# Kernel tuning notes

Hardware: AMD Instinct MI355X
Metric: run time of the kernel (lower is better)

Reference implementation:

```python
import jax, jax.numpy as jnp
import numpy as np

N = 50000
NEG_SLOPE = 0.2


def add_self_loops(edge_index, n):
    loop = jnp.arange(n, dtype=edge_index.dtype)
    return jnp.concatenate([edge_index, jnp.stack([loop, loop])], axis=1)


def gatv2_conv(x, edge_index, Wl, bl, Wr, br, att, bias):
    """PyG GATv2Conv (share_weights=False, concat=True, add_self_loops applied by caller).
    x: [N, Fin]; edge_index: [2, E] with row0=src(j), row1=dst(i); att: [H, D].
    Returns (out [N, H*D], alpha [E, H])."""
    src, dst = edge_index[0], edge_index[1]
    H, D = att.shape
    n = x.shape[0]
    xl = (x @ Wl + bl).reshape(n, H, D)   # source-side transform
    xr = (x @ Wr + br).reshape(n, H, D)   # target-side transform
    e = jax.nn.leaky_relu(xl[src] + xr[dst], NEG_SLOPE)        # [E, H, D]
    logit = jnp.einsum('ehd,hd->eh', e, att)                    # [E, H]
    # segment softmax over edges grouped by target node
    lmax = jax.ops.segment_max(logit, dst, num_segments=n)      # [N, H]
    ex = jnp.exp(logit - lmax[dst])
    denom = jax.ops.segment_sum(ex, dst, num_segments=n)
    alpha = ex / denom[dst]                                     # [E, H]
    out = jax.ops.segment_sum(alpha[:, :, None] * xl[src], dst, num_segments=n)  # [N, H, D]
    return out.reshape(n, H * D) + bias, alpha


def setup_inputs() -> dict:
    key = jax.random.key(0)
    ks = jax.random.split(key, 16)
    E = 400000
    x = jax.random.normal(ks[0], (N, 23), dtype=jnp.float32)
    edge_index = jax.random.randint(ks[1], (2, E), 0, N, dtype=jnp.int64)
    H1, D1 = 8, 64
    F1 = H1 * D1  # 512
    s = 0.1
    return {
        'x': x,
        'edge_index': edge_index,
        'Wl1': jax.random.normal(ks[2], (23, F1), dtype=jnp.float32) * s,
        'bl1': jnp.zeros((F1,), jnp.float32),
        'Wr1': jax.random.normal(ks[3], (23, F1), dtype=jnp.float32) * s,
        'br1': jnp.zeros((F1,), jnp.float32),
        'att1': jax.random.normal(ks[4], (H1, D1), dtype=jnp.float32) * s,
        'bias1': jnp.zeros((F1,), jnp.float32),
        'Wl2': jax.random.normal(ks[5], (F1, 1), dtype=jnp.float32) * s,
        'bl2': jnp.zeros((1,), jnp.float32),
        'Wr2': jax.random.normal(ks[6], (F1, 1), dtype=jnp.float32) * s,
        'br2': jnp.zeros((1,), jnp.float32),
        'att2': jax.random.normal(ks[7], (1, 1), dtype=jnp.float32) * s,
        'bias2': jnp.zeros((1,), jnp.float32),
    }


def reference(x, edge_index, Wl1, bl1, Wr1, br1, att1, bias1,
              Wl2, bl2, Wr2, br2, att2, bias2):
    ei = add_self_loops(edge_index, N)
    h, _ = gatv2_conv(x, ei, Wl1, bl1, Wr1, br1, att1, bias1)
    h = jax.nn.relu(h)
    h, alpha = gatv2_conv(h, ei, Wl2, bl2, Wr2, br2, att2, bias2)
    return h, alpha
```

## Files before the change

### kernel.cpp

```cpp
#include <hip/hip_runtime.h>
#include <math.h>

#define NN 50000
#define E0 400000
#define EE 450000
#define FF 512
#define G1 2048
#define NPB 25
#define EPB 220
#define WAVES_TOTAL (G1 * 4)
#define MAXD 64
#define LOG2E 1.44269504f

typedef _Float16 h2 __attribute__((ext_vector_type(2)));

__device__ __forceinline__ h2 uas_h2(unsigned u) { union { unsigned u; h2 h; } c; c.u = u; return c.h; }
__device__ __forceinline__ unsigned h2as_u(h2 h) { union { unsigned u; h2 h; } c; c.h = h; return c.u; }
__device__ __forceinline__ unsigned packh(float a, float b) {
    h2 hh = { (_Float16)a, (_Float16)b };
    return h2as_u(hh);
}
__device__ __forceinline__ float leaky(float v) { return fmaxf(v, 0.2f * v); }

template<int CTRL>
__device__ __forceinline__ float dppadd(float v) {
    int s = __builtin_amdgcn_update_dpp(0, __float_as_int(v), CTRL, 0xF, 0xF, true);
    return v + __int_as_float(s);
}

__global__ __launch_bounds__(256) void k_predeg(
    const float* __restrict__ x,
    const float* __restrict__ Wl1, const float* __restrict__ bl1,
    const float* __restrict__ Wr1, const float* __restrict__ br1,
    const int* __restrict__ ei,
    unsigned short* __restrict__ xlq, float* __restrict__ xlsc,
    unsigned* __restrict__ xrh,
    int* __restrict__ cnt, int* __restrict__ src_sl)
{
    __shared__ unsigned sxh[NPB * 12];
    __shared__ float swm[2][4];
    int b = blockIdx.x, t = threadIdx.x;
    int l = t & 63, w = t >> 6;

    {
        int e0 = b * EPB;
        int e1 = e0 + EPB; if (e1 > EE) e1 = EE;
        for (int e = e0 + t; e < e1; e += 256) {
            int src, dst;
            if (e < E0) { src = ei[e]; dst = ei[E0 + e]; }
            else        { src = e - E0; dst = src; }
            int p = atomicAdd(&cnt[dst], 1);
            if (p < MAXD) src_sl[(size_t)dst * MAXD + p] = src;
        }
    }

    int i0 = b * NPB;
    int i1 = i0 + NPB; if (i1 > NN) i1 = NN;
    int nnod = i1 - i0;
    for (int k = t; k < nnod * 12; k += 256) {
        int n = k / 12, j = k - n * 12;
        const float* row = x + (size_t)(i0 + n) * 23;
        float f0 = row[2 * j];
        float f1 = (2 * j + 1 < 23) ? row[2 * j + 1] : 0.f;
        sxh[n * 12 + j] = packh(f0, f1);
    }

    int c0 = 2 * t, c1 = 2 * t + 1;
    h2 wl0[12], wl1[12], wr0[12], wr1[12];
#pragma unroll
    for (int j = 0; j < 12; j++) {
        int r0 = 2 * j, r1 = 2 * j + 1;
        float a, b2;
        a = Wl1[r0 * FF + c0]; b2 = (r1 < 23) ? Wl1[r1 * FF + c0] : 0.f;
        wl0[j] = (h2){ (_Float16)a, (_Float16)b2 };
        a = Wl1[r0 * FF + c1]; b2 = (r1 < 23) ? Wl1[r1 * FF + c1] : 0.f;
        wl1[j] = (h2){ (_Float16)a, (_Float16)b2 };
        a = Wr1[r0 * FF + c0]; b2 = (r1 < 23) ? Wr1[r1 * FF + c0] : 0.f;
        wr0[j] = (h2){ (_Float16)a, (_Float16)b2 };
        a = Wr1[r0 * FF + c1]; b2 = (r1 < 23) ? Wr1[r1 * FF + c1] : 0.f;
        wr1[j] = (h2){ (_Float16)a, (_Float16)b2 };
    }
    float bl0 = bl1[c0], bl1s = bl1[c1];
    float br0 = br1[c0], br1s = br1[c1];
    __syncthreads();

    const uint4* S = (const uint4*)sxh;
    for (int n = 0; n < nnod; n++) {
        uint4 xa = S[n * 3 + 0];
        uint4 xb = S[n * 3 + 1];
        uint4 xc = S[n * 3 + 2];
        h2 xv[12] = { uas_h2(xa.x), uas_h2(xa.y), uas_h2(xa.z), uas_h2(xa.w),
                      uas_h2(xb.x), uas_h2(xb.y), uas_h2(xb.z), uas_h2(xb.w),
                      uas_h2(xc.x), uas_h2(xc.y), uas_h2(xc.z), uas_h2(xc.w) };
        float al0 = bl0, al1 = bl1s, ar0 = br0, ar1 = br1s;
#pragma unroll
        for (int j = 0; j < 12; j++) {
            al0 = __builtin_amdgcn_fdot2(wl0[j], xv[j], al0, false);
            al1 = __builtin_amdgcn_fdot2(wl1[j], xv[j], al1, false);
            ar0 = __builtin_amdgcn_fdot2(wr0[j], xv[j], ar0, false);
            ar1 = __builtin_amdgcn_fdot2(wr1[j], xv[j], ar1, false);
        }
        xrh[(size_t)(i0 + n) * 256 + t] = packh(ar0, ar1);
        float ml = fmaxf(fabsf(al0), fabsf(al1));
#pragma unroll
        for (int o = 32; o > 0; o >>= 1) ml = fmaxf(ml, __shfl_xor(ml, o, 64));
        if (l == 0) swm[n & 1][w] = ml;
        __syncthreads();
        float rml = fmaxf(fmaxf(swm[n & 1][0], swm[n & 1][1]),
                          fmaxf(swm[n & 1][2], swm[n & 1][3]));
        rml = fmaxf(rml, 1e-8f);
        float qil = 127.f / rml;
        int q0 = (int)rintf(fminf(fmaxf(al0 * qil, -127.f), 127.f)) + 128;
        int q1 = (int)rintf(fminf(fmaxf(al1 * qil, -127.f), 127.f)) + 128;
        xlq[(size_t)(i0 + n) * 256 + t] =
            (unsigned short)((q0 & 0xFF) | ((q1 & 0xFF) << 8));
        if (t == 0) xlsc[i0 + n] = rml * (1.f / 127.f);
    }
}

__global__ __launch_bounds__(256) void k_layer1(
    const unsigned char* __restrict__ xlq, const float* __restrict__ xlsc,
    const uint4* __restrict__ xrh,
    const float* __restrict__ att, const float* __restrict__ bias1,
    const float* __restrict__ Wl2, const float* __restrict__ bl2,
    const float* __restrict__ Wr2, const float* __restrict__ br2,
    const int* __restrict__ cnt, const int* __restrict__ src_sl,
    float* __restrict__ xl2, float* __restrict__ xr2)
{
    int t = threadIdx.x;
    int l = t & 63;
    int wid = blockIdx.x * 4 + (t >> 6);

    float4 atA = ((const float4*)att)[2 * l];
    float4 atB = ((const float4*)att)[2 * l + 1];
    h2 a6_0 = { (_Float16)(0.6f * LOG2E * atA.x), (_Float16)(0.6f * LOG2E * atA.y) };
    h2 a6_1 = { (_Float16)(0.6f * LOG2E * atA.z), (_Float16)(0.6f * LOG2E * atA.w) };
    h2 a6_2 = { (_Float16)(0.6f * LOG2E * atB.x), (_Float16)(0.6f * LOG2E * atB.y) };
    h2 a6_3 = { (_Float16)(0.6f * LOG2E * atB.z), (_Float16)(0.6f * LOG2E * atB.w) };
    h2 a4_0 = { (_Float16)(0.4f * LOG2E * atA.x), (_Float16)(0.4f * LOG2E * atA.y) };
    h2 a4_1 = { (_Float16)(0.4f * LOG2E * atA.z), (_Float16)(0.4f * LOG2E * atA.w) };
    h2 a4_2 = { (_Float16)(0.4f * LOG2E * atB.x), (_Float16)(0.4f * LOG2E * atB.y) };
    h2 a4_3 = { (_Float16)(0.4f * LOG2E * atB.z), (_Float16)(0.4f * LOG2E * atB.w) };
    const h2 cm1152 = { (_Float16)(-1152.f), (_Float16)(-1152.f) };
    float bl2v = bl2[0], br2v = br2[0];

    for (int i = wid; i < NN; i += WAVES_TOTAL) {
        uint4 xq = xrh[(size_t)i * 64 + l];
        h2 xp0 = uas_h2(xq.x), xp1 = uas_h2(xq.y), xp2 = uas_h2(xq.z), xp3 = uas_h2(xq.w);

        float s = 0.f;
        h2 A0 = { 0, 0 }, A1 = { 0, 0 }, A2 = { 0, 0 }, A3 = { 0, 0 };

        int dg = cnt[i]; if (dg > MAXD) dg = MAXD;
        int myj = (l < dg) ? src_sl[(size_t)i * MAXD + l] : 0;

        int j0 = __builtin_amdgcn_readlane(myj, 0);
        uint2 r0 = *(const uint2*)(xlq + (size_t)j0 * 512 + 8 * l);
        float S0 = xlsc[j0];
        uint2 r1 = r0; float S1 = S0;
        if (dg > 1) {
            int j1 = __builtin_amdgcn_readlane(myj, 1);
            r1 = *(const uint2*)(xlq + (size_t)j1 * 512 + 8 * l);
            S1 = xlsc[j1];
        }

        for (int p = 0; p < dg; p++) {
            uint2 rn = r0; float Sn = S0;
            if (p + 2 < dg) {
                int jn = __builtin_amdgcn_readlane(myj, p + 2);
                rn = *(const uint2*)(xlq + (size_t)jn * 512 + 8 * l);
                Sn = xlsc[jn];
            }

            unsigned w0u = __builtin_amdgcn_perm(r0.x, 0x64646464u, 0x00050004u);
            unsigned w1u = __builtin_amdgcn_perm(r0.x, 0x64646464u, 0x00070006u);
            unsigned w2u = __builtin_amdgcn_perm(r0.y, 0x64646464u, 0x00050004u);
            unsigned w3u = __builtin_amdgcn_perm(r0.y, 0x64646464u, 0x00070006u);
            h2 qq0 = uas_h2(w0u) + cm1152, qq1 = uas_h2(w1u) + cm1152;
            h2 qq2 = uas_h2(w2u) + cm1152, qq3 = uas_h2(w3u) + cm1152;
            _Float16 Sh = (_Float16)S0;
            h2 Ss = { Sh, Sh };
            h2 v0 = qq0 * Ss, v1 = qq1 * Ss, v2 = qq2 * Ss, v3 = qq3 * Ss;
            h2 t0 = v0 + xp0, t1 = v1 + xp1, t2 = v2 + xp2, t3 = v3 + xp3;
            h2 b0 = uas_h2(h2as_u(t0) & 0x7fff7fffu);
            h2 b1 = uas_h2(h2as_u(t1) & 0x7fff7fffu);
            h2 b2 = uas_h2(h2as_u(t2) & 0x7fff7fffu);
            h2 b3 = uas_h2(h2as_u(t3) & 0x7fff7fffu);
            float part = 0.f;
            part = __builtin_amdgcn_fdot2(a6_0, t0, part, false);
            part = __builtin_amdgcn_fdot2(a4_0, b0, part, false);
            part = __builtin_amdgcn_fdot2(a6_1, t1, part, false);
            part = __builtin_amdgcn_fdot2(a4_1, b1, part, false);
            part = __builtin_amdgcn_fdot2(a6_2, t2, part, false);
            part = __builtin_amdgcn_fdot2(a4_2, b2, part, false);
            part = __builtin_amdgcn_fdot2(a6_3, t3, part, false);
            part = __builtin_amdgcn_fdot2(a4_3, b3, part, false);
            part = dppadd<0xB1>(part);
            part = dppadd<0x4E>(part);
            part = dppadd<0x141>(part);
            float wv = exp2f(part);
            s += wv;
            _Float16 wh = (_Float16)wv;
            h2 w2h = { wh, wh };
            A0 += w2h * v0;
            A1 += w2h * v1;
            A2 += w2h * v2;
            A3 += w2h * v3;
            r0 = r1; S0 = S1; r1 = rn; S1 = Sn;
        }

        float inv = 1.f / s;
        float4 bA = ((const float4*)bias1)[2 * l];
        float4 bB = ((const float4*)bias1)[2 * l + 1];
        float h0 = fmaxf(fmaf((float)A0[0], inv, bA.x), 0.f);
        float h1 = fmaxf(fmaf((float)A0[1], inv, bA.y), 0.f);
        float h2v = fmaxf(fmaf((float)A1[0], inv, bA.z), 0.f);
        float h3 = fmaxf(fmaf((float)A1[1], inv, bA.w), 0.f);
        float h4 = fmaxf(fmaf((float)A2[0], inv, bB.x), 0.f);
        float h5 = fmaxf(fmaf((float)A2[1], inv, bB.y), 0.f);
        float h6 = fmaxf(fmaf((float)A3[0], inv, bB.z), 0.f);
        float h7 = fmaxf(fmaf((float)A3[1], inv, bB.w), 0.f);

        float4 wlA = ((const float4*)Wl2)[2 * l];
        float4 wlB = ((const float4*)Wl2)[2 * l + 1];
        float4 wrA = ((const float4*)Wr2)[2 * l];
        float4 wrB = ((const float4*)Wr2)[2 * l + 1];
        float pl = h0 * wlA.x + h1 * wlA.y + h2v * wlA.z + h3 * wlA.w
                 + h4 * wlB.x + h5 * wlB.y + h6 * wlB.z + h7 * wlB.w;
        float pr = h0 * wrA.x + h1 * wrA.y + h2v * wrA.z + h3 * wrA.w
                 + h4 * wrB.x + h5 * wrB.y + h6 * wrB.z + h7 * wrB.w;
        pl = dppadd<0xB1>(pl);  pr = dppadd<0xB1>(pr);
        pl = dppadd<0x4E>(pl);  pr = dppadd<0x4E>(pr);
        pl = dppadd<0x141>(pl); pr = dppadd<0x141>(pr);
        pl = dppadd<0x140>(pl); pr = dppadd<0x140>(pr);
        pl += __shfl_xor(pl, 16, 64);  pr += __shfl_xor(pr, 16, 64);
        pl += __shfl_xor(pl, 32, 64);  pr += __shfl_xor(pr, 32, 64);
        if (l == 0) {
            xl2[i] = pl + bl2v;
            xr2[i] = pr + br2v;
        }
    }
}

__global__ void k_layer2a(const float* __restrict__ xl2, const float* __restrict__ xr2,
                          const float* __restrict__ att2, const float* __restrict__ bias2,
                          const int* __restrict__ cnt, const int* __restrict__ src_sl,
                          float* __restrict__ out, float* __restrict__ invs)
{
    int i = blockIdx.x * blockDim.x + threadIdx.x;
    if (i >= NN) return;
    int dg = cnt[i]; if (dg > MAXD) dg = MAXD;
    const int* sp = src_sl + (size_t)i * MAXD;
    float xri = xr2[i];
    float a2l = att2[0] * LOG2E;
    float s = 0.f, num = 0.f;
    for (int p = 0; p < dg; p++) {
        float v = xl2[sp[p]];
        float w = exp2f(leaky(v + xri) * a2l);
        s += w;
        num = fmaf(w, v, num);
    }
    out[i] = num / s + bias2[0];
    invs[i] = 1.f / s;
}

__global__ void k_layer2b(const float* __restrict__ xl2, const float* __restrict__ xr2,
                          const float* __restrict__ att2, const int* __restrict__ ei,
                          const float* __restrict__ invs, float* __restrict__ out)
{
    int e = blockIdx.x * blockDim.x + threadIdx.x;
    if (e >= EE) return;
    int src, dst;
    if (e < E0) { src = ei[e]; dst = ei[E0 + e]; }
    else        { src = e - E0; dst = src; }
    float a2l = att2[0] * LOG2E;
    float lg = leaky(xl2[src] + xr2[dst]) * a2l;
    out[NN + e] = exp2f(lg) * invs[dst];
}

extern "C" void kernel_launch(void* const* d_in, const int* in_sizes, int n_in,
                              void* d_out, int out_size, void* d_ws, size_t ws_size,
                              hipStream_t stream)
{
    const float* x     = (const float*)d_in[0];
    const int*   ei    = (const int*)d_in[1];
    const float* Wl1   = (const float*)d_in[2];
    const float* bl1   = (const float*)d_in[3];
    const float* Wr1   = (const float*)d_in[4];
    const float* br1   = (const float*)d_in[5];
    const float* att1  = (const float*)d_in[6];
    const float* bias1 = (const float*)d_in[7];
    const float* Wl2   = (const float*)d_in[8];
    const float* bl2   = (const float*)d_in[9];
    const float* Wr2   = (const float*)d_in[10];
    const float* br2   = (const float*)d_in[11];
    const float* att2  = (const float*)d_in[12];
    const float* bias2 = (const float*)d_in[13];
    float* out = (float*)d_out;

    char* ws = (char*)d_ws;
    unsigned short* xlq = (unsigned short*)ws; ws += (size_t)NN * 512;
    float* xlsc    = (float*)ws;    ws += (size_t)NN * 4;
    unsigned* xrh  = (unsigned*)ws; ws += (size_t)NN * 256 * 4;
    float* xl2     = (float*)ws;    ws += (size_t)NN * 4;
    float* xr2     = (float*)ws;    ws += (size_t)NN * 4;
    float* invs    = (float*)ws;    ws += (size_t)NN * 4;
    int* cnt       = (int*)ws;      ws += (size_t)NN * 4;
    int* src_sl    = (int*)ws;      ws += (size_t)NN * MAXD * 4;

    hipMemsetAsync(cnt, 0, (size_t)NN * 4, stream);

    k_predeg<<<G1, 256, 0, stream>>>(x, Wl1, bl1, Wr1, br1, ei, xlq, xlsc, xrh,
                                     cnt, src_sl);
    k_layer1<<<G1, 256, 0, stream>>>((const unsigned char*)xlq, xlsc,
                                     (const uint4*)xrh,
                                     att1, bias1, Wl2, bl2, Wr2, br2,
                                     cnt, src_sl, xl2, xr2);
    k_layer2a<<<(NN + 255) / 256, 256, 0, stream>>>(xl2, xr2, att2, bias2,
                                                    cnt, src_sl, out, invs);
    k_layer2b<<<(EE + 255) / 256, 256, 0, stream>>>(xl2, xr2, att2, ei, invs, out);
}
```

Measured before the change: 238.0 us.

## Batch per-node quantization sync, deepen gather prefetch, fold dequant into FMA

In the pre-degree kernel, the per-node __syncthreads used for the absmax reduction is replaced by a single barrier after all nodes. The unquantized fp16 values and per-wave maxima are staged in shared memory and quantized in a second pass. In layer1 the neighbour-row prefetch goes from two rows ahead to three, to hide more gather latency. The int8 dequantization (q-1152)*S is folded into one packed FMA q*S + (-1152*S). This costs about 25 KB of extra LDS per block and more registers, and the fp16 rounding of the folded constant slightly changes numerics.

```diff
diff --git a/kernel.cpp b/kernel.cpp
--- a/kernel.cpp
+++ b/kernel.cpp
@@ -38,7 +38,8 @@
     int* __restrict__ cnt, int* __restrict__ src_sl)
 {
     __shared__ unsigned sxh[NPB * 12];
-    __shared__ float swm[2][4];
+    __shared__ unsigned sal[NPB * 256];
+    __shared__ float swm[NPB * 4];
     int b = blockIdx.x, t = threadIdx.x;
     int l = t & 63, w = t >> 6;
 
@@ -101,20 +102,25 @@
             ar1 = __builtin_amdgcn_fdot2(wr1[j], xv[j], ar1, false);
         }
         xrh[(size_t)(i0 + n) * 256 + t] = packh(ar0, ar1);
+        sal[n * 256 + t] = packh(al0, al1);
         float ml = fmaxf(fabsf(al0), fabsf(al1));
 #pragma unroll
         for (int o = 32; o > 0; o >>= 1) ml = fmaxf(ml, __shfl_xor(ml, o, 64));
-        if (l == 0) swm[n & 1][w] = ml;
-        __syncthreads();
-        float rml = fmaxf(fmaxf(swm[n & 1][0], swm[n & 1][1]),
-                          fmaxf(swm[n & 1][2], swm[n & 1][3]));
-        rml = fmaxf(rml, 1e-8f);
-        float qil = 127.f / rml;
-        int q0 = (int)rintf(fminf(fmaxf(al0 * qil, -127.f), 127.f)) + 128;
-        int q1 = (int)rintf(fminf(fmaxf(al1 * qil, -127.f), 127.f)) + 128;
+        if (l == 0) swm[n * 4 + w] = ml;
+    }
+    __syncthreads();
+
+    for (int n = 0; n < nnod; n++) {
+        float rm = fmaxf(fmaxf(swm[n * 4 + 0], swm[n * 4 + 1]),
+                         fmaxf(swm[n * 4 + 2], swm[n * 4 + 3]));
+        rm = fmaxf(rm, 1e-8f);
+        float qi = 127.f / rm;
+        h2 alp = uas_h2(sal[n * 256 + t]);
+        int q0 = (int)rintf(fminf(fmaxf((float)alp[0] * qi, -127.f), 127.f)) + 128;
+        int q1 = (int)rintf(fminf(fmaxf((float)alp[1] * qi, -127.f), 127.f)) + 128;
         xlq[(size_t)(i0 + n) * 256 + t] =
             (unsigned short)((q0 & 0xFF) | ((q1 & 0xFF) << 8));
-        if (t == 0) xlsc[i0 + n] = rml * (1.f / 127.f);
+        if (t == 0) xlsc[i0 + n] = rm * (1.f / 127.f);
     }
 }
 
@@ -141,7 +147,6 @@
     h2 a4_1 = { (_Float16)(0.4f * LOG2E * atA.z), (_Float16)(0.4f * LOG2E * atA.w) };
     h2 a4_2 = { (_Float16)(0.4f * LOG2E * atB.x), (_Float16)(0.4f * LOG2E * atB.y) };
     h2 a4_3 = { (_Float16)(0.4f * LOG2E * atB.z), (_Float16)(0.4f * LOG2E * atB.w) };
-    const h2 cm1152 = { (_Float16)(-1152.f), (_Float16)(-1152.f) };
     float bl2v = bl2[0], br2v = br2[0];
 
     for (int i = wid; i < NN; i += WAVES_TOTAL) {
@@ -157,17 +162,17 @@
         int j0 = __builtin_amdgcn_readlane(myj, 0);
         uint2 r0 = *(const uint2*)(xlq + (size_t)j0 * 512 + 8 * l);
         float S0 = xlsc[j0];
-        uint2 r1 = r0; float S1 = S0;
-        if (dg > 1) {
-            int j1 = __builtin_amdgcn_readlane(myj, 1);
-            r1 = *(const uint2*)(xlq + (size_t)j1 * 512 + 8 * l);
-            S1 = xlsc[j1];
-        }
+        uint2 r1 = r0, r2 = r0;
+        float S1 = S0, S2 = S0;
+        if (dg > 1) { int j = __builtin_amdgcn_readlane(myj, 1);
+                      r1 = *(const uint2*)(xlq + (size_t)j * 512 + 8 * l); S1 = xlsc[j]; }
+        if (dg > 2) { int j = __builtin_amdgcn_readlane(myj, 2);
+                      r2 = *(const uint2*)(xlq + (size_t)j * 512 + 8 * l); S2 = xlsc[j]; }
 
         for (int p = 0; p < dg; p++) {
             uint2 rn = r0; float Sn = S0;
-            if (p + 2 < dg) {
-                int jn = __builtin_amdgcn_readlane(myj, p + 2);
+            if (p + 3 < dg) {
+                int jn = __builtin_amdgcn_readlane(myj, p + 3);
                 rn = *(const uint2*)(xlq + (size_t)jn * 512 + 8 * l);
                 Sn = xlsc[jn];
             }
@@ -176,11 +181,14 @@
             unsigned w1u = __builtin_amdgcn_perm(r0.x, 0x64646464u, 0x00070006u);
             unsigned w2u = __builtin_amdgcn_perm(r0.y, 0x64646464u, 0x00050004u);
             unsigned w3u = __builtin_amdgcn_perm(r0.y, 0x64646464u, 0x00070006u);
-            h2 qq0 = uas_h2(w0u) + cm1152, qq1 = uas_h2(w1u) + cm1152;
-            h2 qq2 = uas_h2(w2u) + cm1152, qq3 = uas_h2(w3u) + cm1152;
             _Float16 Sh = (_Float16)S0;
+            _Float16 Ch = (_Float16)(-1152.f * S0);
             h2 Ss = { Sh, Sh };
-            h2 v0 = qq0 * Ss, v1 = qq1 * Ss, v2 = qq2 * Ss, v3 = qq3 * Ss;
+            h2 Cs = { Ch, Ch };
+            h2 v0 = uas_h2(w0u) * Ss + Cs;
+            h2 v1 = uas_h2(w1u) * Ss + Cs;
+            h2 v2 = uas_h2(w2u) * Ss + Cs;
+            h2 v3 = uas_h2(w3u) * Ss + Cs;
             h2 t0 = v0 + xp0, t1 = v1 + xp1, t2 = v2 + xp2, t3 = v3 + xp3;
             h2 b0 = uas_h2(h2as_u(t0) & 0x7fff7fffu);
             h2 b1 = uas_h2(h2as_u(t1) & 0x7fff7fffu);
@@ -206,7 +214,7 @@
             A1 += w2h * v1;
             A2 += w2h * v2;
             A3 += w2h * v3;
-            r0 = r1; S0 = S1; r1 = rn; S1 = Sn;
+            r0 = r1; S0 = S1; r1 = r2; S1 = S2; r2 = rn; S2 = Sn;
         }
 
         float inv = 1.f / s;
```

Result: no change. 234.9 us (-1.3%).
